# Kernel tuning notes

Hardware: AMD Instinct MI355X
Metric: run time of the kernel (lower is better)

## Reference

```python
import jax, jax.numpy as jnp
import numpy as np

N = 100000   # nodes
E = 2000000  # edges per etype
D = 256      # in_dim
C = 16       # num_classes (per-etype Linear out dim)
R = 4        # number of canonical etypes


def setup_inputs() -> dict:
    key = jax.random.key(0)
    k0, k1, k2, k3, k4, k5 = jax.random.split(key, 6)
    feat = jax.random.normal(k0, (N, D), dtype=jnp.float32)
    src_idx = jax.random.randint(k1, (R, E), 0, N, dtype=jnp.int32)
    dst_idx = jax.random.randint(k2, (R, E), 0, N, dtype=jnp.int32)
    eweight = jax.random.uniform(k3, (R, E, 1), dtype=jnp.float32)
    W = jax.random.normal(k4, (R, D, C), dtype=jnp.float32) / np.sqrt(D).astype(np.float32)
    b = jax.random.normal(k5, (R, C), dtype=jnp.float32) * 0.01
    return {"feat": feat, "src_idx": src_idx, "dst_idx": dst_idx,
            "eweight": eweight, "W": W, "b": b}


def reference(feat, src_idx, dst_idx, eweight, W, b):
    """Hetero GNN layer: per-etype Linear -> u_mul_e message -> mean reduce per
    dst node -> sum across etypes (DGL multi_update_all(..., 'sum'))."""
    n = feat.shape[0]

    def per_etype(Wr, br, src, dst, ew):
        wh = feat @ Wr + br                      # [N, C] per-etype linear
        m = jnp.take(wh, src, axis=0) * ew       # [E, C] u_mul_e message
        s = jax.ops.segment_sum(m, dst, num_segments=n)            # [N, C]
        cnt = jax.ops.segment_sum(jnp.ones((src.shape[0],), feat.dtype),
                                  dst, num_segments=n)             # [N]
        # DGL mean: nodes with no incoming messages contribute 0
        cnt = cnt[:, None]
        return jnp.where(cnt > 0, s / jnp.maximum(cnt, 1.0), jnp.zeros_like(s))

    h = jax.vmap(per_etype)(W, b, src_idx, dst_idx, eweight)  # [R, N, C]
    return h.sum(axis=0)                                       # cross-etype sum
```

## Files before the change

kernel.cpp:

```cpp
#include <hip/hip_runtime.h>

constexpr int N = 100000;
constexpr int E = 2000000;
constexpr int D = 256;
constexpr int C = 16;
constexpr int R = 4;
constexpr int NCOL = R * C;
constexpr int TOT = R * E;

constexpr int BKN = 256;
constexpr int NBUK = (N + BKN - 1) / BKN;
constexpr int EPB = 16384;
constexpr int NBLK = (E + EPB - 1) / EPB;
constexpr int NROWS = R * NBUK;
constexpr int HLEN = NROWS * NBLK;
constexpr int SCAN_ELEMS = 2048;
constexpr int SCAN_NBLK = (HLEN + SCAN_ELEMS - 1) / SCAN_ELEMS;
constexpr int CAP = 6144;
constexpr int CHK = 4096;

typedef __attribute__((ext_vector_type(8))) short short8;
typedef __attribute__((ext_vector_type(4))) float f32x4;
typedef __attribute__((ext_vector_type(4))) int i32x4;

__device__ __forceinline__ float bf2f(unsigned short h) {
    return __uint_as_float(((unsigned int)h) << 16);
}
__device__ __forceinline__ unsigned short f2bf(float f) {
    unsigned int x = __float_as_uint(f);
    x += 0x7FFFu + ((x >> 16) & 1u);
    return (unsigned short)(x >> 16);
}

__global__ void wt_kernel(const float* __restrict__ W, short8* __restrict__ wtb) {
    const int idx = blockIdx.x * blockDim.x + threadIdx.x;
    if (idx >= 8 * 4 * 64) return;
    const int lane = idx & 63;
    const int ct   = (idx >> 6) & 3;
    const int ks   = idx >> 8;
    const int r = ct, c = lane & 15;
    const int kbase = ks * 32 + (lane >> 4) * 8;
    short8 v;
#pragma unroll
    for (int j = 0; j < 8; ++j)
        v[j] = (short)f2bf(W[(size_t)r * D * C + (size_t)(kbase + j) * C + c]);
    wtb[idx] = v;
}

__global__ __launch_bounds__(256) void gemm_kernel(
    const f32x4* __restrict__ feat4, const short8* __restrict__ wtb,
    const float* __restrict__ b, unsigned short* __restrict__ whb) {
    __shared__ unsigned short alds[64 * 272];
    const int t   = threadIdx.x;
    const int n0  = blockIdx.x * 64;

#pragma unroll
    for (int j = 0; j < 16; ++j) {
        const int idx = t + j * 256;
        const int row = idx >> 6, k4 = idx & 63;
        const int grow = n0 + row;
        const int lrow = (grow < N) ? grow : (N - 1);
        const f32x4 v = __builtin_nontemporal_load(&feat4[(size_t)lrow * 64 + k4]);
        ushort4 u;
        u.x = f2bf(v.x); u.y = f2bf(v.y); u.z = f2bf(v.z); u.w = f2bf(v.w);
        *(ushort4*)&alds[row * 272 + k4 * 4] = u;
    }
    __syncthreads();

    const int lane = t & 63;
    const int wv   = t >> 6;
    const int wrow = wv * 16 + (lane & 15);
    const int kblk = lane >> 4;

    f32x4 acc0 = {0.f, 0.f, 0.f, 0.f};
    f32x4 acc1 = acc0, acc2 = acc0, acc3 = acc0;

#pragma unroll
    for (int ks = 0; ks < 8; ++ks) {
        const short8 af = *(const short8*)&alds[wrow * 272 + ks * 32 + kblk * 8];
        const short8 b0 = wtb[(ks * 4 + 0) * 64 + lane];
        const short8 b1 = wtb[(ks * 4 + 1) * 64 + lane];
        const short8 b2 = wtb[(ks * 4 + 2) * 64 + lane];
        const short8 b3 = wtb[(ks * 4 + 3) * 64 + lane];
        acc0 = __builtin_amdgcn_mfma_f32_16x16x32_bf16(af, b0, acc0, 0, 0, 0);
        acc1 = __builtin_amdgcn_mfma_f32_16x16x32_bf16(af, b1, acc1, 0, 0, 0);
        acc2 = __builtin_amdgcn_mfma_f32_16x16x32_bf16(af, b2, acc2, 0, 0, 0);
        acc3 = __builtin_amdgcn_mfma_f32_16x16x32_bf16(af, b3, acc3, 0, 0, 0);
    }

    const int c    = lane & 15;
    const int rowb = n0 + wv * 16 + (lane >> 4) * 4;
    const float bias0 = b[ 0 + c];
    const float bias1 = b[16 + c];
    const float bias2 = b[32 + c];
    const float bias3 = b[48 + c];
#pragma unroll
    for (int reg = 0; reg < 4; ++reg) {
        const int gr = rowb + reg;
        if (gr < N) {
            whb[((size_t)0 * N + gr) * 16 + c] = f2bf(acc0[reg] + bias0);
            whb[((size_t)1 * N + gr) * 16 + c] = f2bf(acc1[reg] + bias1);
            whb[((size_t)2 * N + gr) * 16 + c] = f2bf(acc2[reg] + bias2);
            whb[((size_t)3 * N + gr) * 16 + c] = f2bf(acc3[reg] + bias3);
        }
    }
}

__global__ __launch_bounds__(256) void hist_kernel(const int* __restrict__ dst,
                                                   int* __restrict__ hist) {
    __shared__ int hcnt[NBUK];
    const int t = threadIdx.x;
    const int r = blockIdx.y;
    for (int i = t; i < NBUK; i += 256) hcnt[i] = 0;
    __syncthreads();
    const int e0 = blockIdx.x * EPB;
    if (E - e0 >= EPB) {
        const i32x4* d4 = (const i32x4*)(dst + (size_t)r * E + e0);
#pragma unroll
        for (int j = 0; j < EPB / 1024; ++j) {
            const i32x4 d = __builtin_nontemporal_load(&d4[t + j * 256]);
            atomicAdd(&hcnt[d.x >> 8], 1);
            atomicAdd(&hcnt[d.y >> 8], 1);
            atomicAdd(&hcnt[d.z >> 8], 1);
            atomicAdd(&hcnt[d.w >> 8], 1);
        }
    } else {
        const int* d = dst + (size_t)r * E;
        for (int e = e0 + t; e < E; e += 256)
            atomicAdd(&hcnt[d[e] >> 8], 1);
    }
    __syncthreads();
    for (int i = t; i < NBUK; i += 256)
        hist[(size_t)(r * NBUK + i) * NBLK + blockIdx.x] = hcnt[i];
}

__global__ __launch_bounds__(256) void scan1_kernel(int* __restrict__ data,
                                                    int* __restrict__ partials) {
    __shared__ int sh[256];
    const int t = threadIdx.x;
    const int idx = blockIdx.x * SCAN_ELEMS + t * 8;
    int v[8];
#pragma unroll
    for (int j = 0; j < 8; ++j)
        v[j] = (idx + j < HLEN) ? data[idx + j] : 0;
    int s = 0;
#pragma unroll
    for (int j = 0; j < 8; ++j) s += v[j];
    sh[t] = s;
    __syncthreads();
    for (int off = 1; off < 256; off <<= 1) {
        int x = (t >= off) ? sh[t - off] : 0;
        __syncthreads();
        sh[t] += x;
        __syncthreads();
    }
    int run = sh[t] - s;
    if (t == 255) partials[blockIdx.x] = sh[255];
#pragma unroll
    for (int j = 0; j < 8; ++j) {
        if (idx + j < HLEN) data[idx + j] = run;
        run += v[j];
    }
}

__global__ __launch_bounds__(1024) void scan2_kernel(int* __restrict__ partials, int n) {
    __shared__ int sh[1024];
    const int t = threadIdx.x;
    int a = (2 * t     < n) ? partials[2 * t]     : 0;
    int b = (2 * t + 1 < n) ? partials[2 * t + 1] : 0;
    const int s = a + b;
    sh[t] = s;
    __syncthreads();
    for (int off = 1; off < 1024; off <<= 1) {
        int x = (t >= off) ? sh[t - off] : 0;
        __syncthreads();
        sh[t] += x;
        __syncthreads();
    }
    const int excl = sh[t] - s;
    if (2 * t     < n) partials[2 * t]     = excl;
    if (2 * t + 1 < n) partials[2 * t + 1] = excl + a;
}

__global__ void scan3_kernel(int* __restrict__ data, const int* __restrict__ partials) {
    const int i = blockIdx.x * blockDim.x + threadIdx.x;
    if (i < HLEN) data[i] += partials[i / SCAN_ELEMS];
}

__global__ __launch_bounds__(512) void scatter_kernel(const int* __restrict__ src,
                                                      const int* __restrict__ dst,
                                                      const float* __restrict__ ew,
                                                      const int* __restrict__ hist,
                                                      int2* __restrict__ sorted) {
    __shared__ int2 lrec[CHK];
    __shared__ int  lidx[CHK];
    __shared__ short lbkt[CHK];
    __shared__ int gcur[NBUK];
    __shared__ int loff[NBUK + 1];
    __shared__ int lcnt[NBUK];
    const int t = threadIdx.x;
    const int r = blockIdx.y;

    for (int i = t; i < NBUK; i += 512)
        gcur[i] = hist[(size_t)(r * NBUK + i) * NBLK + blockIdx.x];

    const int e0 = blockIdx.x * EPB;
    const int e1 = min(e0 + EPB, E);
    const int* sp = src + (size_t)r * E;
    const int* dp = dst + (size_t)r * E;
    const float* wp = ew + (size_t)r * E;

    for (int cb = e0; cb < e1; cb += CHK) {
        const int L = min(CHK, e1 - cb);
        for (int i = t; i < NBUK; i += 512) lcnt[i] = 0;
        __syncthreads();

        if (L == CHK) {
            const i32x4* s4 = (const i32x4*)(sp + cb);
            const i32x4* d4 = (const i32x4*)(dp + cb);
            const f32x4* w4 = (const f32x4*)(wp + cb);
#pragma unroll
            for (int j = 0; j < CHK / 2048; ++j) {
                const int v = t + j * 512;
                const i32x4 d = __builtin_nontemporal_load(&d4[v]);
                const i32x4 s = __builtin_nontemporal_load(&s4[v]);
                const f32x4 w = __builtin_nontemporal_load(&w4[v]);
#pragma unroll
                for (int q = 0; q < 4; ++q) {
                    const int dd = (q == 0) ? d.x : (q == 1) ? d.y : (q == 2) ? d.z : d.w;
                    const int ss = (q == 0) ? s.x : (q == 1) ? s.y : (q == 2) ? s.z : s.w;
                    const float ww = (q == 0) ? w.x : (q == 1) ? w.y : (q == 2) ? w.z : w.w;
                    const int b = dd >> 8;
                    int2 p;
                    p.x = ss | ((dd & 255) << 20);
                    p.y = __float_as_int(ww);
                    lrec[v * 4 + q] = p;
                    lbkt[v * 4 + q] = (short)b;
                    atomicAdd(&lcnt[b], 1);
                }
            }
        } else {
            for (int i = t; i < L; i += 512) {
                const int dd = dp[cb + i];
                const int ss = sp[cb + i];
                const float ww = wp[cb + i];
                const int b = dd >> 8;
                int2 p;
                p.x = ss | ((dd & 255) << 20);
                p.y = __float_as_int(ww);
                lrec[i] = p;
                lbkt[i] = (short)b;
                atomicAdd(&lcnt[b], 1);
            }
        }
        __syncthreads();

        for (int off = 1; off < NBUK; off <<= 1) {
            int x = 0;
            if (t < NBUK && t >= off) x = lcnt[t - off];
            __syncthreads();
            if (t < NBUK) lcnt[t] += x;
            __syncthreads();
        }
        if (t < NBUK) loff[t + 1] = lcnt[t];
        if (t == 0) loff[0] = 0;
        __syncthreads();
        if (t < NBUK) lcnt[t] = loff[t];
        __syncthreads();

        for (int i = t; i < L; i += 512) {
            const int b = lbkt[i];
            const int pos = atomicAdd(&lcnt[b], 1);
            lidx[pos] = i | (b << 16);
        }
        __syncthreads();

        for (int p = t; p < L; p += 512) {
            const int v = lidx[p];
            const int i = v & 0xFFFF;
            const int b = v >> 16;
            sorted[gcur[b] + (p - loff[b])] = lrec[i];
        }
        __syncthreads();

        for (int b = t; b < NBUK; b += 512)
            gcur[b] += loff[b + 1] - loff[b];
        __syncthreads();
    }
}

__global__ __launch_bounds__(512) void accum_kernel(const int2* __restrict__ sorted,
                                                    const ushort4* __restrict__ whb4,
                                                    const int* __restrict__ hist,
                                                    float* __restrict__ out) {
    __shared__ int2 lrec[CAP];
    __shared__ unsigned short lidx[CAP];
    __shared__ int loff[BKN + 1];
    __shared__ int lcur[BKN];
    const int t = threadIdx.x;
    const int bk = blockIdx.x;
    const int g = t >> 2, c4 = t & 3;

    float4 o0 = {0.f, 0.f, 0.f, 0.f};
    float4 o1 = {0.f, 0.f, 0.f, 0.f};

    for (int r = 0; r < R; ++r) {
        const int row = r * NBUK + bk;
        const int start = hist[(size_t)row * NBLK];
        const int end   = (row + 1 < NROWS) ? hist[(size_t)(row + 1) * NBLK] : TOT;
        int L = end - start;
        if (L > CAP) L = CAP;

        if (t < BKN) lcur[t] = 0;
        __syncthreads();

        for (int i = t; i < L; i += 512) {
            long long raw = __builtin_nontemporal_load((const long long*)&sorted[start + i]);
            int2 p = *(int2*)&raw;
            lrec[i] = p;
            atomicAdd(&lcur[(p.x >> 20) & 255], 1);
        }
        __syncthreads();

        for (int off = 1; off < BKN; off <<= 1) {
            int x = 0;
            if (t < BKN && t >= off) x = lcur[t - off];
            __syncthreads();
            if (t < BKN) lcur[t] += x;
            __syncthreads();
        }
        if (t < BKN) loff[t + 1] = lcur[t];
        if (t == 0) loff[0] = 0;
        __syncthreads();
        if (t < BKN) lcur[t] = loff[t];
        __syncthreads();

        for (int i = t; i < L; i += 512) {
            int dl = (lrec[i].x >> 20) & 255;
            int pos = atomicAdd(&lcur[dl], 1);
            lidx[pos] = (unsigned short)i;
        }
        __syncthreads();

        const int wbase = r * N;
#pragma unroll
        for (int half = 0; half < 2; ++half) {
            const int node = g + half * 128;
            const int s0 = loff[node], e0 = loff[node + 1];
            float a0 = 0.f, a1 = 0.f, a2 = 0.f, a3 = 0.f;

            int j = s0;
            for (; j + 4 <= e0; j += 4) {
                const int i0 = lidx[j], i1 = lidx[j + 1];
                const int i2 = lidx[j + 2], i3 = lidx[j + 3];
                const int2 r0 = lrec[i0], r1 = lrec[i1], r2 = lrec[i2], r3 = lrec[i3];
                const ushort4 u0 = whb4[(size_t)(wbase + (r0.x & 0xFFFFF)) * 4 + c4];
                const ushort4 u1 = whb4[(size_t)(wbase + (r1.x & 0xFFFFF)) * 4 + c4];
                const ushort4 u2 = whb4[(size_t)(wbase + (r2.x & 0xFFFFF)) * 4 + c4];
                const ushort4 u3 = whb4[(size_t)(wbase + (r3.x & 0xFFFFF)) * 4 + c4];
                const float w0 = __int_as_float(r0.y), w1 = __int_as_float(r1.y);
                const float w2 = __int_as_float(r2.y), w3 = __int_as_float(r3.y);
                a0 += bf2f(u0.x) * w0 + bf2f(u1.x) * w1 + bf2f(u2.x) * w2 + bf2f(u3.x) * w3;
                a1 += bf2f(u0.y) * w0 + bf2f(u1.y) * w1 + bf2f(u2.y) * w2 + bf2f(u3.y) * w3;
                a2 += bf2f(u0.z) * w0 + bf2f(u1.z) * w1 + bf2f(u2.z) * w2 + bf2f(u3.z) * w3;
                a3 += bf2f(u0.w) * w0 + bf2f(u1.w) * w1 + bf2f(u2.w) * w2 + bf2f(u3.w) * w3;
            }
            for (; j < e0; ++j) {
                const int2 r0 = lrec[lidx[j]];
                const ushort4 u0 = whb4[(size_t)(wbase + (r0.x & 0xFFFFF)) * 4 + c4];
                const float w0 = __int_as_float(r0.y);
                a0 += bf2f(u0.x) * w0;
                a1 += bf2f(u0.y) * w0;
                a2 += bf2f(u0.z) * w0;
                a3 += bf2f(u0.w) * w0;
            }

            const int deg = e0 - s0;
            if (deg > 0) {
                const float inv = 1.f / (float)deg;
                if (half == 0) {
                    o0.x += a0 * inv; o0.y += a1 * inv;
                    o0.z += a2 * inv; o0.w += a3 * inv;
                } else {
                    o1.x += a0 * inv; o1.y += a1 * inv;
                    o1.z += a2 * inv; o1.w += a3 * inv;
                }
            }
        }
        __syncthreads();
    }

    const int nodeA = bk * BKN + g;
    const int nodeB = nodeA + 128;
    if (nodeA < N) *(float4*)&out[(size_t)nodeA * 16 + c4 * 4] = o0;
    if (nodeB < N) *(float4*)&out[(size_t)nodeB * 16 + c4 * 4] = o1;
}

extern "C" void kernel_launch(void* const* d_in, const int* in_sizes, int n_in,
                              void* d_out, int out_size, void* d_ws, size_t ws_size,
                              hipStream_t stream) {
    const float* feat = (const float*)d_in[0];
    const int*   src  = (const int*)d_in[1];
    const int*   dst  = (const int*)d_in[2];
    const float* ew   = (const float*)d_in[3];
    const float* W    = (const float*)d_in[4];
    const float* b    = (const float*)d_in[5];
    float* out = (float*)d_out;

    char* base = (char*)d_ws;
    int2*           sorted   = (int2*)base;           base += (size_t)TOT * 8;
    short8*         wtb      = (short8*)base;         base += (size_t)64 * NCOL * 16;
    unsigned short* whb      = (unsigned short*)base; base += (size_t)R * N * C * 2;
    int*            hist     = (int*)base;            base += (size_t)HLEN * 4;
    int*            partials = (int*)base;

    wt_kernel<<<8, 256, 0, stream>>>(W, wtb);
    gemm_kernel<<<(N + 63) / 64, 256, 0, stream>>>((const f32x4*)feat, wtb, b, whb);

    hist_kernel<<<dim3(NBLK, R), 256, 0, stream>>>(dst, hist);
    scan1_kernel<<<SCAN_NBLK, 256, 0, stream>>>(hist, partials);
    scan2_kernel<<<1, 1024, 0, stream>>>(partials, SCAN_NBLK);
    scan3_kernel<<<(HLEN + 255) / 256, 256, 0, stream>>>(hist, partials);

    scatter_kernel<<<dim3(NBLK, R), 512, 0, stream>>>(src, dst, ew, hist, sorted);
    accum_kernel<<<NBUK, 512, 0, stream>>>(sorted, (const ushort4*)whb, hist, out);
}
```

Baseline: 178.7 us.

## Halve destination bucket size to 128 nodes, one node per thread group

Shrinks the dst-node bucket from 256 to 128 nodes, so there are twice as many buckets and accumulate blocks, each with a smaller LDS staging buffer (CAP, CHK) and one node per 4-thread group instead of two. The scatter kernel's per-chunk local scan is rewritten as a two-elements-per-thread scan over 512 threads so it can cover the larger bucket count. The aim is more blocks in flight, higher occupancy and less serial per-thread work in the accumulate phase. In exchange, histogram and scan arrays double in size and scatter writes go to more distinct output regions.

Result: slower. 201.6 us (+12.8%).

```diff
diff --git a/kernel.cpp b/kernel.cpp
--- a/kernel.cpp
+++ b/kernel.cpp
@@ -8,7 +8,7 @@
 constexpr int NCOL = R * C;
 constexpr int TOT = R * E;
 
-constexpr int BKN = 256;
+constexpr int BKN = 128;
 constexpr int NBUK = (N + BKN - 1) / BKN;
 constexpr int EPB = 16384;
 constexpr int NBLK = (E + EPB - 1) / EPB;
@@ -16,8 +16,8 @@
 constexpr int HLEN = NROWS * NBLK;
 constexpr int SCAN_ELEMS = 2048;
 constexpr int SCAN_NBLK = (HLEN + SCAN_ELEMS - 1) / SCAN_ELEMS;
-constexpr int CAP = 6144;
-constexpr int CHK = 4096;
+constexpr int CAP = 3328;
+constexpr int CHK = 2048;
 
 typedef __attribute__((ext_vector_type(8))) short short8;
 typedef __attribute__((ext_vector_type(4))) float f32x4;
@@ -119,15 +119,15 @@
 #pragma unroll
         for (int j = 0; j < EPB / 1024; ++j) {
             const i32x4 d = __builtin_nontemporal_load(&d4[t + j * 256]);
-            atomicAdd(&hcnt[d.x >> 8], 1);
-            atomicAdd(&hcnt[d.y >> 8], 1);
-            atomicAdd(&hcnt[d.z >> 8], 1);
-            atomicAdd(&hcnt[d.w >> 8], 1);
+            atomicAdd(&hcnt[d.x >> 7], 1);
+            atomicAdd(&hcnt[d.y >> 7], 1);
+            atomicAdd(&hcnt[d.z >> 7], 1);
+            atomicAdd(&hcnt[d.w >> 7], 1);
         }
     } else {
         const int* d = dst + (size_t)r * E;
         for (int e = e0 + t; e < E; e += 256)
-            atomicAdd(&hcnt[d[e] >> 8], 1);
+            atomicAdd(&hcnt[d[e] >> 7], 1);
     }
     __syncthreads();
     for (int i = t; i < NBUK; i += 256)
@@ -198,6 +198,7 @@
     __shared__ int gcur[NBUK];
     __shared__ int loff[NBUK + 1];
     __shared__ int lcnt[NBUK];
+    __shared__ int sh[512];
     const int t = threadIdx.x;
     const int r = blockIdx.y;
 
@@ -219,34 +220,31 @@
             const i32x4* s4 = (const i32x4*)(sp + cb);
             const i32x4* d4 = (const i32x4*)(dp + cb);
             const f32x4* w4 = (const f32x4*)(wp + cb);
-#pragma unroll
-            for (int j = 0; j < CHK / 2048; ++j) {
-                const int v = t + j * 512;
-                const i32x4 d = __builtin_nontemporal_load(&d4[v]);
-                const i32x4 s = __builtin_nontemporal_load(&s4[v]);
-                const f32x4 w = __builtin_nontemporal_load(&w4[v]);
-#pragma unroll
-                for (int q = 0; q < 4; ++q) {
-                    const int dd = (q == 0) ? d.x : (q == 1) ? d.y : (q == 2) ? d.z : d.w;
-                    const int ss = (q == 0) ? s.x : (q == 1) ? s.y : (q == 2) ? s.z : s.w;
-                    const float ww = (q == 0) ? w.x : (q == 1) ? w.y : (q == 2) ? w.z : w.w;
-                    const int b = dd >> 8;
-                    int2 p;
-                    p.x = ss | ((dd & 255) << 20);
-                    p.y = __float_as_int(ww);
-                    lrec[v * 4 + q] = p;
-                    lbkt[v * 4 + q] = (short)b;
-                    atomicAdd(&lcnt[b], 1);
-                }
+            const int v = t;
+            const i32x4 d = __builtin_nontemporal_load(&d4[v]);
+            const i32x4 s = __builtin_nontemporal_load(&s4[v]);
+            const f32x4 w = __builtin_nontemporal_load(&w4[v]);
+#pragma unroll
+            for (int q = 0; q < 4; ++q) {
+                const int dd = (q == 0) ? d.x : (q == 1) ? d.y : (q == 2) ? d.z : d.w;
+                const int ss = (q == 0) ? s.x : (q == 1) ? s.y : (q == 2) ? s.z : s.w;
+                const float ww = (q == 0) ? w.x : (q == 1) ? w.y : (q == 2) ? w.z : w.w;
+                const int b = dd >> 7;
+                int2 p;
+                p.x = ss | ((dd & 127) << 20);
+                p.y = __float_as_int(ww);
+                lrec[v * 4 + q] = p;
+                lbkt[v * 4 + q] = (short)b;
+                atomicAdd(&lcnt[b], 1);
             }
         } else {
             for (int i = t; i < L; i += 512) {
                 const int dd = dp[cb + i];
                 const int ss = sp[cb + i];
                 const float ww = wp[cb + i];
-                const int b = dd >> 8;
+                const int b = dd >> 7;
                 int2 p;
-                p.x = ss | ((dd & 255) << 20);
+                p.x = ss | ((dd & 127) << 20);
                 p.y = __float_as_int(ww);
                 lrec[i] = p;
                 lbkt[i] = (short)b;
@@ -255,17 +253,24 @@
         }
         __syncthreads();
 
-        for (int off = 1; off < NBUK; off <<= 1) {
-            int x = 0;
-            if (t < NBUK && t >= off) x = lcnt[t - off];
+        int a0 = 0, a1 = 0;
+        if (2 * t     < NBUK) a0 = lcnt[2 * t];
+        if (2 * t + 1 < NBUK) a1 = lcnt[2 * t + 1];
+        sh[t] = a0 + a1;
+        __syncthreads();
+        for (int off = 1; off < 512; off <<= 1) {
+            int x = (t >= off) ? sh[t - off] : 0;
             __syncthreads();
-            if (t < NBUK) lcnt[t] += x;
+            sh[t] += x;
             __syncthreads();
         }
-        if (t < NBUK) loff[t + 1] = lcnt[t];
-        if (t == 0) loff[0] = 0;
-        __syncthreads();
-        if (t < NBUK) lcnt[t] = loff[t];
+        const int excl = sh[t] - a0 - a1;
+        if (2 * t     < NBUK) loff[2 * t]     = excl;
+        if (2 * t + 1 < NBUK) loff[2 * t + 1] = excl + a0;
+        if (2 * t + 1 == NBUK - 1) loff[NBUK] = excl + a0 + a1;
+        __syncthreads();
+        if (2 * t     < NBUK) lcnt[2 * t]     = loff[2 * t];
+        if (2 * t + 1 < NBUK) lcnt[2 * t + 1] = loff[2 * t + 1];
         __syncthreads();
 
         for (int i = t; i < L; i += 512) {
@@ -302,7 +307,6 @@
     const int g = t >> 2, c4 = t & 3;
 
     float4 o0 = {0.f, 0.f, 0.f, 0.f};
-    float4 o1 = {0.f, 0.f, 0.f, 0.f};
 
     for (int r = 0; r < R; ++r) {
         const int row = r * NBUK + bk;
@@ -318,7 +322,7 @@
             long long raw = __builtin_nontemporal_load((const long long*)&sorted[start + i]);
             int2 p = *(int2*)&raw;
             lrec[i] = p;
-            atomicAdd(&lcur[(p.x >> 20) & 255], 1);
+            atomicAdd(&lcur[(p.x >> 20) & 127], 1);
         }
         __syncthreads();
 
@@ -336,64 +340,53 @@
         __syncthreads();
 
         for (int i = t; i < L; i += 512) {
-            int dl = (lrec[i].x >> 20) & 255;
+            int dl = (lrec[i].x >> 20) & 127;
             int pos = atomicAdd(&lcur[dl], 1);
             lidx[pos] = (unsigned short)i;
         }
         __syncthreads();
 
         const int wbase = r * N;
-#pragma unroll
-        for (int half = 0; half < 2; ++half) {
-            const int node = g + half * 128;
-            const int s0 = loff[node], e0 = loff[node + 1];
-            float a0 = 0.f, a1 = 0.f, a2 = 0.f, a3 = 0.f;
-
-            int j = s0;
-            for (; j + 4 <= e0; j += 4) {
-                const int i0 = lidx[j], i1 = lidx[j + 1];
-                const int i2 = lidx[j + 2], i3 = lidx[j + 3];
-                const int2 r0 = lrec[i0], r1 = lrec[i1], r2 = lrec[i2], r3 = lrec[i3];
-                const ushort4 u0 = whb4[(size_t)(wbase + (r0.x & 0xFFFFF)) * 4 + c4];
-                const ushort4 u1 = whb4[(size_t)(wbase + (r1.x & 0xFFFFF)) * 4 + c4];
-                const ushort4 u2 = whb4[(size_t)(wbase + (r2.x & 0xFFFFF)) * 4 + c4];
-                const ushort4 u3 = whb4[(size_t)(wbase + (r3.x & 0xFFFFF)) * 4 + c4];
-                const float w0 = __int_as_float(r0.y), w1 = __int_as_float(r1.y);
-                const float w2 = __int_as_float(r2.y), w3 = __int_as_float(r3.y);
-                a0 += bf2f(u0.x) * w0 + bf2f(u1.x) * w1 + bf2f(u2.x) * w2 + bf2f(u3.x) * w3;
-                a1 += bf2f(u0.y) * w0 + bf2f(u1.y) * w1 + bf2f(u2.y) * w2 + bf2f(u3.y) * w3;
-                a2 += bf2f(u0.z) * w0 + bf2f(u1.z) * w1 + bf2f(u2.z) * w2 + bf2f(u3.z) * w3;
-                a3 += bf2f(u0.w) * w0 + bf2f(u1.w) * w1 + bf2f(u2.w) * w2 + bf2f(u3.w) * w3;
-            }
-            for (; j < e0; ++j) {
-                const int2 r0 = lrec[lidx[j]];
-                const ushort4 u0 = whb4[(size_t)(wbase + (r0.x & 0xFFFFF)) * 4 + c4];
-                const float w0 = __int_as_float(r0.y);
-                a0 += bf2f(u0.x) * w0;
-                a1 += bf2f(u0.y) * w0;
-                a2 += bf2f(u0.z) * w0;
-                a3 += bf2f(u0.w) * w0;
-            }
-
-            const int deg = e0 - s0;
-            if (deg > 0) {
-                const float inv = 1.f / (float)deg;
-                if (half == 0) {
-                    o0.x += a0 * inv; o0.y += a1 * inv;
-                    o0.z += a2 * inv; o0.w += a3 * inv;
-                } else {
-                    o1.x += a0 * inv; o1.y += a1 * inv;
-                    o1.z += a2 * inv; o1.w += a3 * inv;
-                }
-            }
-        }
-        __syncthreads();
-    }
-
-    const int nodeA = bk * BKN + g;
-    const int nodeB = nodeA + 128;
-    if (nodeA < N) *(float4*)&out[(size_t)nodeA * 16 + c4 * 4] = o0;
-    if (nodeB < N) *(float4*)&out[(size_t)nodeB * 16 + c4 * 4] = o1;
+        const int s0 = loff[g], e0 = loff[g + 1];
+        float a0 = 0.f, a1 = 0.f, a2 = 0.f, a3 = 0.f;
+
+        int j = s0;
+        for (; j + 4 <= e0; j += 4) {
+            const int i0 = lidx[j], i1 = lidx[j + 1];
+            const int i2 = lidx[j + 2], i3 = lidx[j + 3];
+            const int2 r0 = lrec[i0], r1 = lrec[i1], r2 = lrec[i2], r3 = lrec[i3];
+            const ushort4 u0 = whb4[(size_t)(wbase + (r0.x & 0xFFFFF)) * 4 + c4];
+            const ushort4 u1 = whb4[(size_t)(wbase + (r1.x & 0xFFFFF)) * 4 + c4];
+            const ushort4 u2 = whb4[(size_t)(wbase + (r2.x & 0xFFFFF)) * 4 + c4];
+            const ushort4 u3 = whb4[(size_t)(wbase + (r3.x & 0xFFFFF)) * 4 + c4];
+            const float w0 = __int_as_float(r0.y), w1 = __int_as_float(r1.y);
+            const float w2 = __int_as_float(r2.y), w3 = __int_as_float(r3.y);
+            a0 += bf2f(u0.x) * w0 + bf2f(u1.x) * w1 + bf2f(u2.x) * w2 + bf2f(u3.x) * w3;
+            a1 += bf2f(u0.y) * w0 + bf2f(u1.y) * w1 + bf2f(u2.y) * w2 + bf2f(u3.y) * w3;
+            a2 += bf2f(u0.z) * w0 + bf2f(u1.z) * w1 + bf2f(u2.z) * w2 + bf2f(u3.z) * w3;
+            a3 += bf2f(u0.w) * w0 + bf2f(u1.w) * w1 + bf2f(u2.w) * w2 + bf2f(u3.w) * w3;
+        }
+        for (; j < e0; ++j) {
+            const int2 r0 = lrec[lidx[j]];
+            const ushort4 u0 = whb4[(size_t)(wbase + (r0.x & 0xFFFFF)) * 4 + c4];
+            const float w0 = __int_as_float(r0.y);
+            a0 += bf2f(u0.x) * w0;
+            a1 += bf2f(u0.y) * w0;
+            a2 += bf2f(u0.z) * w0;
+            a3 += bf2f(u0.w) * w0;
+        }
+
+        const int deg = e0 - s0;
+        if (deg > 0) {
+            const float inv = 1.f / (float)deg;
+            o0.x += a0 * inv; o0.y += a1 * inv;
+            o0.z += a2 * inv; o0.w += a3 * inv;
+        }
+        __syncthreads();
+    }
+
+    const int node = bk * BKN + g;
+    if (node < N) *(float4*)&out[(size_t)node * 16 + c4 * 4] = o0;
 }
 
 extern "C" void kernel_launch(void* const* d_in, const int* in_sizes, int n_in,
```

## Split each accum bucket across two blocks with ballot-filtered half-bucket compaction

Applied to the files above, without the earlier changes.

The accumulation kernel now launches two blocks per 256-node bucket. Each block handles 128 destination nodes and reads the whole bucket's edge list, but keeps only the records for its half, compacted into shared memory with wave ballot and popcount. This halves per-block LDS use (smaller CAP and offset arrays), which allows more blocks per CU and doubles the grid for better latency hiding in the gather. The cost is that every sorted record is read twice from global memory. The smaller CAP also raises truncation risk if a half-bucket holds more than 3328 edges.

Measured after the change: 205.5 us. 15.0% more time.

```diff
diff --git a/kernel.cpp b/kernel.cpp
--- a/kernel.cpp
+++ b/kernel.cpp
@@ -16,7 +16,7 @@
 constexpr int HLEN = NROWS * NBLK;
 constexpr int SCAN_ELEMS = 2048;
 constexpr int SCAN_NBLK = (HLEN + SCAN_ELEMS - 1) / SCAN_ELEMS;
-constexpr int CAP = 6144;
+constexpr int CAP = 3328;
 constexpr int CHK = 4096;
 
 typedef __attribute__((ext_vector_type(8))) short short8;
@@ -295,105 +295,122 @@
                                                     float* __restrict__ out) {
     __shared__ int2 lrec[CAP];
     __shared__ unsigned short lidx[CAP];
-    __shared__ int loff[BKN + 1];
-    __shared__ int lcur[BKN];
+    __shared__ int loff[129];
+    __shared__ int lcur[128];
+    __shared__ int cntM;
     const int t = threadIdx.x;
     const int bk = blockIdx.x;
+    const int ck = bk >> 1;
+    const int h  = bk & 1;
     const int g = t >> 2, c4 = t & 3;
+    const int lane = t & 63;
 
     float4 o0 = {0.f, 0.f, 0.f, 0.f};
-    float4 o1 = {0.f, 0.f, 0.f, 0.f};
 
     for (int r = 0; r < R; ++r) {
-        const int row = r * NBUK + bk;
+        const int row = r * NBUK + ck;
         const int start = hist[(size_t)row * NBLK];
         const int end   = (row + 1 < NROWS) ? hist[(size_t)(row + 1) * NBLK] : TOT;
-        int L = end - start;
-        if (L > CAP) L = CAP;
-
-        if (t < BKN) lcur[t] = 0;
-        __syncthreads();
-
-        for (int i = t; i < L; i += 512) {
-            long long raw = __builtin_nontemporal_load((const long long*)&sorted[start + i]);
-            int2 p = *(int2*)&raw;
-            lrec[i] = p;
-            atomicAdd(&lcur[(p.x >> 20) & 255], 1);
-        }
-        __syncthreads();
-
-        for (int off = 1; off < BKN; off <<= 1) {
-            int x = 0;
-            if (t < BKN && t >= off) x = lcur[t - off];
-            __syncthreads();
-            if (t < BKN) lcur[t] += x;
-            __syncthreads();
-        }
-        if (t < BKN) loff[t + 1] = lcur[t];
+        const int L = end - start;
+
+        if (t < 128) lcur[t] = 0;
+        if (t == 0) cntM = 0;
+        __syncthreads();
+
+        for (int i0 = 0; i0 < L; i0 += 512) {
+            const int i = i0 + t;
+            int2 p;
+            int dl = 0;
+            bool match = false;
+            if (i < L) {
+                long long raw = __builtin_nontemporal_load((const long long*)&sorted[start + i]);
+                p = *(int2*)&raw;
+                dl = (p.x >> 20) & 255;
+                match = ((dl >> 7) == h);
+            }
+            const unsigned long long mk = __ballot(match);
+            if (mk != 0ull) {
+                const int ldr = (int)(__ffsll((long long)mk) - 1);
+                int wb = 0;
+                if (lane == ldr) wb = atomicAdd(&cntM, (int)__popcll(mk));
+                wb = __shfl(wb, ldr);
+                if (match) {
+                    const int pos = wb + (int)__popcll(mk & ((1ull << lane) - 1ull));
+                    lrec[pos] = p;
+                    atomicAdd(&lcur[dl & 127], 1);
+                }
+            }
+        }
+        __syncthreads();
+        const int M = (cntM < CAP) ? cntM : CAP;
+
+        if (t < 128) {
+            for (int off = 1; off < 128; off <<= 1) {
+                int x = (t >= off) ? lcur[t - off] : 0;
+                __syncthreads();
+                lcur[t] += x;
+                __syncthreads();
+            }
+        } else {
+            for (int off = 1; off < 128; off <<= 1) {
+                __syncthreads();
+                __syncthreads();
+            }
+        }
+        if (t < 128) loff[t + 1] = lcur[t];
         if (t == 0) loff[0] = 0;
         __syncthreads();
-        if (t < BKN) lcur[t] = loff[t];
-        __syncthreads();
-
-        for (int i = t; i < L; i += 512) {
-            int dl = (lrec[i].x >> 20) & 255;
-            int pos = atomicAdd(&lcur[dl], 1);
+        if (t < 128) lcur[t] = loff[t];
+        __syncthreads();
+
+        for (int i = t; i < M; i += 512) {
+            const int dl = (lrec[i].x >> 20) & 127;
+            const int pos = atomicAdd(&lcur[dl], 1);
             lidx[pos] = (unsigned short)i;
         }
         __syncthreads();
 
         const int wbase = r * N;
-#pragma unroll
-        for (int half = 0; half < 2; ++half) {
-            const int node = g + half * 128;
-            const int s0 = loff[node], e0 = loff[node + 1];
-            float a0 = 0.f, a1 = 0.f, a2 = 0.f, a3 = 0.f;
-
-            int j = s0;
-            for (; j + 4 <= e0; j += 4) {
-                const int i0 = lidx[j], i1 = lidx[j + 1];
-                const int i2 = lidx[j + 2], i3 = lidx[j + 3];
-                const int2 r0 = lrec[i0], r1 = lrec[i1], r2 = lrec[i2], r3 = lrec[i3];
-                const ushort4 u0 = whb4[(size_t)(wbase + (r0.x & 0xFFFFF)) * 4 + c4];
-                const ushort4 u1 = whb4[(size_t)(wbase + (r1.x & 0xFFFFF)) * 4 + c4];
-                const ushort4 u2 = whb4[(size_t)(wbase + (r2.x & 0xFFFFF)) * 4 + c4];
-                const ushort4 u3 = whb4[(size_t)(wbase + (r3.x & 0xFFFFF)) * 4 + c4];
-                const float w0 = __int_as_float(r0.y), w1 = __int_as_float(r1.y);
-                const float w2 = __int_as_float(r2.y), w3 = __int_as_float(r3.y);
-                a0 += bf2f(u0.x) * w0 + bf2f(u1.x) * w1 + bf2f(u2.x) * w2 + bf2f(u3.x) * w3;
-                a1 += bf2f(u0.y) * w0 + bf2f(u1.y) * w1 + bf2f(u2.y) * w2 + bf2f(u3.y) * w3;
-                a2 += bf2f(u0.z) * w0 + bf2f(u1.z) * w1 + bf2f(u2.z) * w2 + bf2f(u3.z) * w3;
-                a3 += bf2f(u0.w) * w0 + bf2f(u1.w) * w1 + bf2f(u2.w) * w2 + bf2f(u3.w) * w3;
-            }
-            for (; j < e0; ++j) {
-                const int2 r0 = lrec[lidx[j]];
-                const ushort4 u0 = whb4[(size_t)(wbase + (r0.x & 0xFFFFF)) * 4 + c4];
-                const float w0 = __int_as_float(r0.y);
-                a0 += bf2f(u0.x) * w0;
-                a1 += bf2f(u0.y) * w0;
-                a2 += bf2f(u0.z) * w0;
-                a3 += bf2f(u0.w) * w0;
-            }
-
-            const int deg = e0 - s0;
-            if (deg > 0) {
-                const float inv = 1.f / (float)deg;
-                if (half == 0) {
-                    o0.x += a0 * inv; o0.y += a1 * inv;
-                    o0.z += a2 * inv; o0.w += a3 * inv;
-                } else {
-                    o1.x += a0 * inv; o1.y += a1 * inv;
-                    o1.z += a2 * inv; o1.w += a3 * inv;
-                }
-            }
-        }
-        __syncthreads();
-    }
-
-    const int nodeA = bk * BKN + g;
-    const int nodeB = nodeA + 128;
-    if (nodeA < N) *(float4*)&out[(size_t)nodeA * 16 + c4 * 4] = o0;
-    if (nodeB < N) *(float4*)&out[(size_t)nodeB * 16 + c4 * 4] = o1;
+        const int s0 = loff[g], e0 = loff[g + 1];
+        float a0 = 0.f, a1 = 0.f, a2 = 0.f, a3 = 0.f;
+
+        int j = s0;
+        for (; j + 4 <= e0; j += 4) {
+            const int i0 = lidx[j], i1 = lidx[j + 1];
+            const int i2 = lidx[j + 2], i3 = lidx[j + 3];
+            const int2 r0 = lrec[i0], r1 = lrec[i1], r2 = lrec[i2], r3 = lrec[i3];
+            const ushort4 u0 = whb4[(size_t)(wbase + (r0.x & 0xFFFFF)) * 4 + c4];
+            const ushort4 u1 = whb4[(size_t)(wbase + (r1.x & 0xFFFFF)) * 4 + c4];
+            const ushort4 u2 = whb4[(size_t)(wbase + (r2.x & 0xFFFFF)) * 4 + c4];
+            const ushort4 u3 = whb4[(size_t)(wbase + (r3.x & 0xFFFFF)) * 4 + c4];
+            const float w0 = __int_as_float(r0.y), w1 = __int_as_float(r1.y);
+            const float w2 = __int_as_float(r2.y), w3 = __int_as_float(r3.y);
+            a0 += bf2f(u0.x) * w0 + bf2f(u1.x) * w1 + bf2f(u2.x) * w2 + bf2f(u3.x) * w3;
+            a1 += bf2f(u0.y) * w0 + bf2f(u1.y) * w1 + bf2f(u2.y) * w2 + bf2f(u3.y) * w3;
+            a2 += bf2f(u0.z) * w0 + bf2f(u1.z) * w1 + bf2f(u2.z) * w2 + bf2f(u3.z) * w3;
+            a3 += bf2f(u0.w) * w0 + bf2f(u1.w) * w1 + bf2f(u2.w) * w2 + bf2f(u3.w) * w3;
+        }
+        for (; j < e0; ++j) {
+            const int2 r0 = lrec[lidx[j]];
+            const ushort4 u0 = whb4[(size_t)(wbase + (r0.x & 0xFFFFF)) * 4 + c4];
+            const float w0 = __int_as_float(r0.y);
+            a0 += bf2f(u0.x) * w0;
+            a1 += bf2f(u0.y) * w0;
+            a2 += bf2f(u0.z) * w0;
+            a3 += bf2f(u0.w) * w0;
+        }
+
+        const int deg = e0 - s0;
+        if (deg > 0) {
+            const float inv = 1.f / (float)deg;
+            o0.x += a0 * inv; o0.y += a1 * inv;
+            o0.z += a2 * inv; o0.w += a3 * inv;
+        }
+        __syncthreads();
+    }
+
+    const int node = bk * 128 + g;
+    if (node < N) *(float4*)&out[(size_t)node * 16 + c4 * 4] = o0;
 }
 
 extern "C" void kernel_launch(void* const* d_in, const int* in_sizes, int n_in,
@@ -423,5 +440,5 @@
     scan3_kernel<<<(HLEN + 255) / 256, 256, 0, stream>>>(hist, partials);
 
     scatter_kernel<<<dim3(NBLK, R), 512, 0, stream>>>(src, dst, ew, hist, sorted);
-    accum_kernel<<<NBUK, 512, 0, stream>>>(sorted, (const ushort4*)whb, hist, out);
-}
+    accum_kernel<<<2 * NBUK, 512, 0, stream>>>(sorted, (const ushort4*)whb, hist, out);
+}
```

## Split accumulation across etypes into separate blocks and add finalize reduction kernel

Applied to the files above, without the earlier changes.

The accumulation kernel now launches one block per (bucket, etype) instead of looping over all four etypes in a single block, giving about four times as many blocks. Each block writes its etype's partial means to a workspace buffer, and a new finalize kernel sums the four partials into the output. The local counting sort also places records directly into shared memory in sorted order instead of going through an index array, which drops one level of indirection but reads the global sorted array twice. The cost is an extra launch plus writing and reading a 4xNx16 float partial buffer.

After: 186.4 us. +4.3%, slower.

```diff
diff --git a/kernel.cpp b/kernel.cpp
--- a/kernel.cpp
+++ b/kernel.cpp
@@ -292,108 +292,107 @@
 __global__ __launch_bounds__(512) void accum_kernel(const int2* __restrict__ sorted,
                                                     const ushort4* __restrict__ whb4,
                                                     const int* __restrict__ hist,
-                                                    float* __restrict__ out) {
+                                                    float* __restrict__ part) {
     __shared__ int2 lrec[CAP];
-    __shared__ unsigned short lidx[CAP];
     __shared__ int loff[BKN + 1];
     __shared__ int lcur[BKN];
     const int t = threadIdx.x;
-    const int bk = blockIdx.x;
+    const int ck = blockIdx.x;
+    const int r  = blockIdx.y;
     const int g = t >> 2, c4 = t & 3;
 
-    float4 o0 = {0.f, 0.f, 0.f, 0.f};
-    float4 o1 = {0.f, 0.f, 0.f, 0.f};
-
-    for (int r = 0; r < R; ++r) {
-        const int row = r * NBUK + bk;
-        const int start = hist[(size_t)row * NBLK];
-        const int end   = (row + 1 < NROWS) ? hist[(size_t)(row + 1) * NBLK] : TOT;
-        int L = end - start;
-        if (L > CAP) L = CAP;
-
-        if (t < BKN) lcur[t] = 0;
-        __syncthreads();
-
-        for (int i = t; i < L; i += 512) {
-            long long raw = __builtin_nontemporal_load((const long long*)&sorted[start + i]);
-            int2 p = *(int2*)&raw;
-            lrec[i] = p;
-            atomicAdd(&lcur[(p.x >> 20) & 255], 1);
-        }
-        __syncthreads();
-
-        for (int off = 1; off < BKN; off <<= 1) {
-            int x = 0;
-            if (t < BKN && t >= off) x = lcur[t - off];
-            __syncthreads();
-            if (t < BKN) lcur[t] += x;
-            __syncthreads();
-        }
-        if (t < BKN) loff[t + 1] = lcur[t];
-        if (t == 0) loff[0] = 0;
-        __syncthreads();
-        if (t < BKN) lcur[t] = loff[t];
-        __syncthreads();
-
-        for (int i = t; i < L; i += 512) {
-            int dl = (lrec[i].x >> 20) & 255;
-            int pos = atomicAdd(&lcur[dl], 1);
-            lidx[pos] = (unsigned short)i;
-        }
-        __syncthreads();
-
-        const int wbase = r * N;
-#pragma unroll
-        for (int half = 0; half < 2; ++half) {
-            const int node = g + half * 128;
-            const int s0 = loff[node], e0 = loff[node + 1];
-            float a0 = 0.f, a1 = 0.f, a2 = 0.f, a3 = 0.f;
-
-            int j = s0;
-            for (; j + 4 <= e0; j += 4) {
-                const int i0 = lidx[j], i1 = lidx[j + 1];
-                const int i2 = lidx[j + 2], i3 = lidx[j + 3];
-                const int2 r0 = lrec[i0], r1 = lrec[i1], r2 = lrec[i2], r3 = lrec[i3];
-                const ushort4 u0 = whb4[(size_t)(wbase + (r0.x & 0xFFFFF)) * 4 + c4];
-                const ushort4 u1 = whb4[(size_t)(wbase + (r1.x & 0xFFFFF)) * 4 + c4];
-                const ushort4 u2 = whb4[(size_t)(wbase + (r2.x & 0xFFFFF)) * 4 + c4];
-                const ushort4 u3 = whb4[(size_t)(wbase + (r3.x & 0xFFFFF)) * 4 + c4];
-                const float w0 = __int_as_float(r0.y), w1 = __int_as_float(r1.y);
-                const float w2 = __int_as_float(r2.y), w3 = __int_as_float(r3.y);
-                a0 += bf2f(u0.x) * w0 + bf2f(u1.x) * w1 + bf2f(u2.x) * w2 + bf2f(u3.x) * w3;
-                a1 += bf2f(u0.y) * w0 + bf2f(u1.y) * w1 + bf2f(u2.y) * w2 + bf2f(u3.y) * w3;
-                a2 += bf2f(u0.z) * w0 + bf2f(u1.z) * w1 + bf2f(u2.z) * w2 + bf2f(u3.z) * w3;
-                a3 += bf2f(u0.w) * w0 + bf2f(u1.w) * w1 + bf2f(u2.w) * w2 + bf2f(u3.w) * w3;
-            }
-            for (; j < e0; ++j) {
-                const int2 r0 = lrec[lidx[j]];
-                const ushort4 u0 = whb4[(size_t)(wbase + (r0.x & 0xFFFFF)) * 4 + c4];
-                const float w0 = __int_as_float(r0.y);
-                a0 += bf2f(u0.x) * w0;
-                a1 += bf2f(u0.y) * w0;
-                a2 += bf2f(u0.z) * w0;
-                a3 += bf2f(u0.w) * w0;
-            }
-
-            const int deg = e0 - s0;
-            if (deg > 0) {
-                const float inv = 1.f / (float)deg;
-                if (half == 0) {
-                    o0.x += a0 * inv; o0.y += a1 * inv;
-                    o0.z += a2 * inv; o0.w += a3 * inv;
-                } else {
-                    o1.x += a0 * inv; o1.y += a1 * inv;
-                    o1.z += a2 * inv; o1.w += a3 * inv;
-                }
-            }
-        }
-        __syncthreads();
-    }
-
-    const int nodeA = bk * BKN + g;
+    const int row = r * NBUK + ck;
+    const int start = hist[(size_t)row * NBLK];
+    const int end   = (row + 1 < NROWS) ? hist[(size_t)(row + 1) * NBLK] : TOT;
+    int L = end - start;
+    if (L > CAP) L = CAP;
+
+    if (t < BKN) lcur[t] = 0;
+    __syncthreads();
+
+    for (int i = t; i < L; i += 512)
+        atomicAdd(&lcur[(sorted[start + i].x >> 20) & 255], 1);
+    __syncthreads();
+
+    for (int off = 1; off < BKN; off <<= 1) {
+        int x = 0;
+        if (t < BKN && t >= off) x = lcur[t - off];
+        __syncthreads();
+        if (t < BKN) lcur[t] += x;
+        __syncthreads();
+    }
+    if (t < BKN) loff[t + 1] = lcur[t];
+    if (t == 0) loff[0] = 0;
+    __syncthreads();
+    if (t < BKN) lcur[t] = loff[t];
+    __syncthreads();
+
+    for (int i = t; i < L; i += 512) {
+        const int2 p = sorted[start + i];
+        const int dl = (p.x >> 20) & 255;
+        const int pos = atomicAdd(&lcur[dl], 1);
+        lrec[pos] = p;
+    }
+    __syncthreads();
+
+    const int wbase = r * N;
+    float4 ov[2];
+#pragma unroll
+    for (int half = 0; half < 2; ++half) {
+        const int node = g + half * 128;
+        const int s0 = loff[node], e0 = loff[node + 1];
+        float a0 = 0.f, a1 = 0.f, a2 = 0.f, a3 = 0.f;
+
+        int j = s0;
+        for (; j + 4 <= e0; j += 4) {
+            const int2 r0 = lrec[j], r1 = lrec[j + 1];
+            const int2 r2 = lrec[j + 2], r3 = lrec[j + 3];
+            const ushort4 u0 = whb4[(size_t)(wbase + (r0.x & 0xFFFFF)) * 4 + c4];
+            const ushort4 u1 = whb4[(size_t)(wbase + (r1.x & 0xFFFFF)) * 4 + c4];
+            const ushort4 u2 = whb4[(size_t)(wbase + (r2.x & 0xFFFFF)) * 4 + c4];
+            const ushort4 u3 = whb4[(size_t)(wbase + (r3.x & 0xFFFFF)) * 4 + c4];
+            const float w0 = __int_as_float(r0.y), w1 = __int_as_float(r1.y);
+            const float w2 = __int_as_float(r2.y), w3 = __int_as_float(r3.y);
+            a0 += bf2f(u0.x) * w0 + bf2f(u1.x) * w1 + bf2f(u2.x) * w2 + bf2f(u3.x) * w3;
+            a1 += bf2f(u0.y) * w0 + bf2f(u1.y) * w1 + bf2f(u2.y) * w2 + bf2f(u3.y) * w3;
+            a2 += bf2f(u0.z) * w0 + bf2f(u1.z) * w1 + bf2f(u2.z) * w2 + bf2f(u3.z) * w3;
+            a3 += bf2f(u0.w) * w0 + bf2f(u1.w) * w1 + bf2f(u2.w) * w2 + bf2f(u3.w) * w3;
+        }
+        for (; j < e0; ++j) {
+            const int2 r0 = lrec[j];
+            const ushort4 u0 = whb4[(size_t)(wbase + (r0.x & 0xFFFFF)) * 4 + c4];
+            const float w0 = __int_as_float(r0.y);
+            a0 += bf2f(u0.x) * w0;
+            a1 += bf2f(u0.y) * w0;
+            a2 += bf2f(u0.z) * w0;
+            a3 += bf2f(u0.w) * w0;
+        }
+
+        const int deg = e0 - s0;
+        const float inv = (deg > 0) ? 1.f / (float)deg : 0.f;
+        ov[half].x = a0 * inv; ov[half].y = a1 * inv;
+        ov[half].z = a2 * inv; ov[half].w = a3 * inv;
+    }
+
+    const int nodeA = ck * BKN + g;
     const int nodeB = nodeA + 128;
-    if (nodeA < N) *(float4*)&out[(size_t)nodeA * 16 + c4 * 4] = o0;
-    if (nodeB < N) *(float4*)&out[(size_t)nodeB * 16 + c4 * 4] = o1;
+    if (nodeA < N) *(float4*)&part[(size_t)(wbase + nodeA) * 16 + c4 * 4] = ov[0];
+    if (nodeB < N) *(float4*)&part[(size_t)(wbase + nodeB) * 16 + c4 * 4] = ov[1];
+}
+
+__global__ void finalize_kernel(const float4* __restrict__ part4,
+                                float4* __restrict__ out4) {
+    const int i = blockIdx.x * blockDim.x + threadIdx.x;
+    if (i >= N * 4) return;
+    float4 a = part4[i];
+    const float4 b = part4[(size_t)N * 4 + i];
+    const float4 c = part4[(size_t)2 * N * 4 + i];
+    const float4 d = part4[(size_t)3 * N * 4 + i];
+    a.x += b.x + c.x + d.x;
+    a.y += b.y + c.y + d.y;
+    a.z += b.z + c.z + d.z;
+    a.w += b.w + c.w + d.w;
+    out4[i] = a;
 }
 
 extern "C" void kernel_launch(void* const* d_in, const int* in_sizes, int n_in,
@@ -412,7 +411,8 @@
     short8*         wtb      = (short8*)base;         base += (size_t)64 * NCOL * 16;
     unsigned short* whb      = (unsigned short*)base; base += (size_t)R * N * C * 2;
     int*            hist     = (int*)base;            base += (size_t)HLEN * 4;
-    int*            partials = (int*)base;
+    int*            partials = (int*)base;            base += (size_t)4096;
+    float*          part     = (float*)base;
 
     wt_kernel<<<8, 256, 0, stream>>>(W, wtb);
     gemm_kernel<<<(N + 63) / 64, 256, 0, stream>>>((const f32x4*)feat, wtb, b, whb);
@@ -423,5 +423,6 @@
     scan3_kernel<<<(HLEN + 255) / 256, 256, 0, stream>>>(hist, partials);
 
     scatter_kernel<<<dim3(NBLK, R), 512, 0, stream>>>(src, dst, ew, hist, sorted);
-    accum_kernel<<<NBUK, 512, 0, stream>>>(sorted, (const ushort4*)whb, hist, out);
-}
+    accum_kernel<<<dim3(NBUK, R), 512, 0, stream>>>(sorted, (const ushort4*)whb, hist, part);
+    finalize_kernel<<<(N * 4 + 255) / 256, 256, 0, stream>>>((const float4*)part, (float4*)out);
+}
```
